# Optimization experiments

Measured on AMD Instinct MI355X. Metric: run time of the kernel, lower is better.

The kernel has to match this reference:

```python
import jax, jax.numpy as jnp
import numpy as np

N = 500_000
E = 16_000_000
G = 5_000
F_IN = 64
DIM = 10


def _mlp(x, W1, b1, W2, b2):
    return jnp.maximum(x @ W1 + b1, 0.0) @ W2 + b2


def setup_inputs() -> dict:
    key = jax.random.key(0)
    ks = jax.random.split(key, 32)
    inp = {
        "h": jax.random.normal(ks[0], (N, F_IN), dtype=jnp.float32),
        "src": jax.random.randint(ks[1], (E,), 0, N, dtype=jnp.int32),
        "dst": jax.random.randint(ks[2], (E,), 0, N, dtype=jnp.int32),
        "node_graph": jnp.sort(jax.random.randint(ks[3], (N,), 0, G, dtype=jnp.int32)),
    }
    k = 4
    for i in range(1, 6):
        d_in = F_IN if i == 1 else DIM
        inp[f"W1_{i}"] = jax.random.normal(ks[k], (d_in, DIM), dtype=jnp.float32) * 0.1; k += 1
        inp[f"b1_{i}"] = jnp.zeros((DIM,), dtype=jnp.float32)
        inp[f"W2_{i}"] = jax.random.normal(ks[k], (DIM, DIM), dtype=jnp.float32) * 0.1; k += 1
        inp[f"b2_{i}"] = jnp.zeros((DIM,), dtype=jnp.float32)
        inp[f"l_{i}"] = jax.random.normal(ks[k], (DIM, 1), dtype=jnp.float32) * 0.1; k += 1
    return inp


def reference(h, src, dst, node_graph,
              W1_1, b1_1, W2_1, b2_1, l_1,
              W1_2, b1_2, W2_2, b2_2, l_2,
              W1_3, b1_3, W2_3, b2_3, l_3,
              W1_4, b1_4, W2_4, b2_4, l_4,
              W1_5, b1_5, W2_5, b2_5, l_5):
    # GINConv with eps=0: out = MLP(h + sum_{j in N(i)} h_j), then outer ReLU
    def gin(x, W1, b1, W2, b2):
        agg = jax.ops.segment_sum(x[src], dst, num_segments=N)
        return jnp.maximum(_mlp(x + agg, W1, b1, W2, b2), 0.0)

    x1 = gin(h, W1_1, b1_1, W2_1, b2_1)
    x2 = gin(x1, W1_2, b1_2, W2_2, b2_2)
    x3 = gin(x2, W1_3, b1_3, W2_3, b2_3)
    x4 = gin(x3, W1_4, b1_4, W2_4, b2_4)
    x5 = gin(x4, W1_5, b1_5, W2_5, b2_5)

    counts = jax.ops.segment_sum(jnp.ones((N,), dtype=jnp.float32), node_graph, num_segments=G)
    counts = jnp.maximum(counts, 1.0)[:, None]  # [G,1]

    def mean_nodes(x):
        return jax.ops.segment_sum(x, node_graph, num_segments=G) / counts

    s = (mean_nodes(x1) @ l_1 + mean_nodes(x2) @ l_2 + mean_nodes(x3) @ l_3
         + mean_nodes(x4) @ l_4 + mean_nodes(x5) @ l_5)  # [G,1]
    return jax.nn.sigmoid(s)
```

## Files before the change

### kernel.cpp

```cpp
#include <hip/hip_runtime.h>


#define SENTINEL 0xFFFFFFFFu

__device__ __forceinline__ unsigned short f2bf(float f) {
    unsigned b = __float_as_uint(f);
    b += 0x7fffu + ((b >> 16) & 1u);
    return (unsigned short)(b >> 16);
}
__device__ __forceinline__ float bflo(unsigned u) { return __uint_as_float(u << 16); }
__device__ __forceinline__ float bfhi(unsigned u) { return __uint_as_float(u & 0xffff0000u); }

__global__ void k1_hw1_bf16(const float* __restrict__ h, const float* __restrict__ W1,
                            unsigned* __restrict__ y, int N) {
    __shared__ float sW[640];
    for (int i = threadIdx.x; i < 640; i += blockDim.x) sW[i] = W1[i];
    __syncthreads();
    int n = blockIdx.x * blockDim.x + threadIdx.x;
    if (n >= N) return;
    const float* hr = h + (size_t)n * 64;
    float acc[10];
#pragma unroll
    for (int j = 0; j < 10; j++) acc[j] = 0.f;
#pragma unroll 4
    for (int k = 0; k < 64; k += 4) {
        float4 hv = *(const float4*)(hr + k);
#pragma unroll
        for (int j = 0; j < 10; j++) {
            acc[j] += hv.x * sW[(k + 0) * 10 + j];
            acc[j] += hv.y * sW[(k + 1) * 10 + j];
            acc[j] += hv.z * sW[(k + 2) * 10 + j];
            acc[j] += hv.w * sW[(k + 3) * 10 + j];
        }
    }
    unsigned r0 = (unsigned)f2bf(acc[0]) | ((unsigned)f2bf(acc[1]) << 16);
    unsigned r1 = (unsigned)f2bf(acc[2]) | ((unsigned)f2bf(acc[3]) << 16);
    unsigned r2 = (unsigned)f2bf(acc[4]) | ((unsigned)f2bf(acc[5]) << 16);
    unsigned r3 = (unsigned)f2bf(acc[6]) | ((unsigned)f2bf(acc[7]) << 16);
    unsigned r4 = (unsigned)f2bf(acc[8]) | ((unsigned)f2bf(acc[9]) << 16);
    unsigned* yr = y + (size_t)n * 8;
    *(uint4*)yr = make_uint4(r0, r1, r2, r3);
    yr[4] = r4;
}

__global__ void k1_hw1_f32(const float* __restrict__ h, const float* __restrict__ W1,
                           float* __restrict__ y, int N) {
    __shared__ float sW[640];
    for (int i = threadIdx.x; i < 640; i += blockDim.x) sW[i] = W1[i];
    __syncthreads();
    int n = blockIdx.x * blockDim.x + threadIdx.x;
    if (n >= N) return;
    const float* hr = h + (size_t)n * 64;
    float acc[10];
#pragma unroll
    for (int j = 0; j < 10; j++) acc[j] = 0.f;
#pragma unroll 4
    for (int k = 0; k < 64; k += 4) {
        float4 hv = *(const float4*)(hr + k);
#pragma unroll
        for (int j = 0; j < 10; j++) {
            acc[j] += hv.x * sW[(k + 0) * 10 + j];
            acc[j] += hv.y * sW[(k + 1) * 10 + j];
            acc[j] += hv.z * sW[(k + 2) * 10 + j];
            acc[j] += hv.w * sW[(k + 3) * 10 + j];
        }
    }
    float* yr = y + (size_t)n * 16;
#pragma unroll
    for (int j = 0; j < 10; j++) yr[j] = acc[j];
}

__global__ void k_bhist(const int* __restrict__ dst, unsigned* __restrict__ bucket_cnt,
                        int E) {
    __shared__ unsigned h[512];
    int t = threadIdx.x;
    h[t] = 0; h[t + 256] = 0;
    __syncthreads();
    int stride = gridDim.x * blockDim.x;
    for (int e = blockIdx.x * blockDim.x + t; e < E; e += stride)
        atomicAdd(&h[(unsigned)dst[e] >> 10], 1u);
    __syncthreads();
    if (h[t]) atomicAdd(&bucket_cnt[t], h[t]);
    if (h[t + 256]) atomicAdd(&bucket_cnt[t + 256], h[t + 256]);
}

__global__ void k_bscan(const unsigned* __restrict__ bucket_cnt,
                        unsigned* __restrict__ bbase, unsigned* __restrict__ bcur, int B) {
    __shared__ unsigned s[512];
    int t = threadIdx.x;
    unsigned v = (t < B) ? bucket_cnt[t] : 0u;
    s[t] = v;
    __syncthreads();
    for (int off = 1; off < 512; off <<= 1) {
        unsigned u = (t >= off) ? s[t - off] : 0u;
        __syncthreads();
        s[t] += u;
        __syncthreads();
    }
    unsigned excl = s[t] - v;
    if (t < B) { bbase[t] = excl; bcur[t] = excl; }
    if (t == B - 1) bbase[B] = s[t];
}

__global__ __launch_bounds__(1024) void k_bscatter2(
        const int* __restrict__ src, const int* __restrict__ dst,
        unsigned* __restrict__ bcur, unsigned* __restrict__ pairs,
        int E, int nblocks) {
    __shared__ unsigned cnt[512];
    int t = threadIdx.x;
    int per = (E + nblocks - 1) / nblocks;
    int beg = blockIdx.x * per;
    int end = beg + per; if (end > E) end = E;
    if (beg >= E) return;
    if (t < 512) cnt[t] = 0;
    __syncthreads();
    for (int e = beg + t; e < end; e += 1024)
        atomicAdd(&cnt[(unsigned)dst[e] >> 10], 1u);
    __syncthreads();
    unsigned c = 0, base = 0;
    if (t < 512) { c = cnt[t]; if (c) base = atomicAdd(&bcur[t], c); }
    __syncthreads();
    if (t < 512) cnt[t] = base;
    __syncthreads();
    for (int e = beg + t; e < end; e += 1024) {
        unsigned d = (unsigned)dst[e];
        unsigned pos = atomicAdd(&cnt[d >> 10], 1u);
        pairs[pos] = ((unsigned)src[e] << 10) | (d & 1023u);
    }
}

__global__ __launch_bounds__(1024) void k_p2(
        const unsigned* __restrict__ pairs, const unsigned* __restrict__ bbase,
        unsigned* __restrict__ edges, unsigned* __restrict__ row_start,
        int N, int B, int E, int packed) {
    __shared__ unsigned cnt[1024], scn[1024], cur[1024];
    int t = threadIdx.x, b = blockIdx.x;
    unsigned beg = bbase[b], end = bbase[b + 1];
    cnt[t] = 0;
    __syncthreads();
    for (unsigned e = beg + t; e < end; e += 1024)
        atomicAdd(&cnt[pairs[e] & 1023u], 1u);
    __syncthreads();
    unsigned v = cnt[t];
    scn[t] = v;
    __syncthreads();
    for (int off = 1; off < 1024; off <<= 1) {
        unsigned u = (t >= off) ? scn[t - off] : 0u;
        __syncthreads();
        scn[t] += u;
        __syncthreads();
    }
    unsigned excl = scn[t] - v;
    int node = (b << 10) + t;
    if (node < N) row_start[node] = beg + excl;
    if (b == B - 1 && t == 0) row_start[N] = (unsigned)E;
    cur[t] = beg + excl;
    __syncthreads();
    for (unsigned e = beg + t; e < end; e += 1024) {
        unsigned pv = pairs[e];
        unsigned pos = atomicAdd(&cur[pv & 1023u], 1u);
        edges[pos] = packed ? pv : (pv >> 10);
    }
}

__global__ __launch_bounds__(256) void kA_agg(
        const unsigned* __restrict__ yin, const unsigned* __restrict__ epk,
        const unsigned* __restrict__ bbase,
        float* __restrict__ agg, float* __restrict__ carry_val,
        unsigned* __restrict__ carry_dst, int E, int B, int W) {
    __shared__ unsigned sb[513];
    for (int i = threadIdx.x; i < B + 1; i += 256) sb[i] = bbase[i];
    __syncthreads();
    int lane = threadIdx.x & 63;
    int w = blockIdx.x * 4 + (threadIdx.x >> 6);
    int e = (w << 6) + lane;
    bool v = e < E;
    float acc[10];
    unsigned dst;
    if (v) {
        unsigned pv = epk[e];
        unsigned s = pv >> 10;
        const unsigned* pr = yin + (size_t)s * 8;
        uint4 q = *(const uint4*)pr;
        unsigned q4 = pr[4];
        int lo = 0, hi = B - 1;
        while (lo < hi) { int m = (lo + hi + 1) >> 1; if (sb[m] <= (unsigned)e) lo = m; else hi = m - 1; }
        dst = ((unsigned)lo << 10) | (pv & 1023u);
        acc[0] = bflo(q.x); acc[1] = bfhi(q.x);
        acc[2] = bflo(q.y); acc[3] = bfhi(q.y);
        acc[4] = bflo(q.z); acc[5] = bfhi(q.z);
        acc[6] = bflo(q.w); acc[7] = bfhi(q.w);
        acc[8] = bflo(q4);  acc[9] = bfhi(q4);
    } else {
        dst = SENTINEL;
#pragma unroll
        for (int j = 0; j < 10; j++) acc[j] = 0.f;
    }
#pragma unroll
    for (int off = 1; off < 64; off <<= 1) {
        unsigned od = __shfl_up(dst, off);
        float tv[10];
#pragma unroll
        for (int j = 0; j < 10; j++) tv[j] = __shfl_up(acc[j], off);
        bool take = (lane >= off) && (od == dst);
#pragma unroll
        for (int j = 0; j < 10; j++) acc[j] = take ? acc[j] + tv[j] : acc[j];
    }
    unsigned dn = __shfl_down(dst, 1);
    bool is_end = (lane < 63) && (dst != dn);
    if (v && is_end) {
        float* ar = agg + (size_t)dst * 16;
        *(float4*)ar = make_float4(acc[0], acc[1], acc[2], acc[3]);
        *(float4*)(ar + 4) = make_float4(acc[4], acc[5], acc[6], acc[7]);
        *(float2*)(ar + 8) = make_float2(acc[8], acc[9]);
    }
    if (lane == 63 && w < W) {
        carry_dst[w] = dst;
        float* cr = carry_val + (size_t)w * 16;
        *(float4*)cr = make_float4(acc[0], acc[1], acc[2], acc[3]);
        *(float4*)(cr + 4) = make_float4(acc[4], acc[5], acc[6], acc[7]);
        *(float2*)(cr + 8) = make_float2(acc[8], acc[9]);
    }
}

__global__ __launch_bounds__(256) void kB_node(
        const unsigned* __restrict__ yin, unsigned* __restrict__ yout,
        const float* __restrict__ agg,
        const unsigned* __restrict__ row_start,
        const unsigned* __restrict__ carry_dst, const float* __restrict__ carry_val,
        const float* __restrict__ b1, const float* __restrict__ W2,
        const float* __restrict__ b2, const float* __restrict__ l,
        const float* __restrict__ W1n,
        const int* __restrict__ node_graph, float* __restrict__ gacc,
        int N, int last) {
    __shared__ float sW2[100], sW1[100], sb1[10], sb2[10], sl[10];
    int t = threadIdx.x;
    if (t < 100) sW2[t] = W2[t];
    if (!last && t >= 128 && t < 228) sW1[t - 128] = W1n[t - 128];
    if (t < 10) { sb1[t] = b1[t]; sb2[t] = b2[t]; sl[t] = l[t]; }
    __syncthreads();
    int n = blockIdx.x * 256 + t;
    bool valid = n < N;
    int nc = valid ? n : (N - 1);
    const unsigned* yr = yin + (size_t)nc * 8;
    uint4 q = *(const uint4*)yr;
    unsigned q4 = yr[4];
    float acc[10] = {bflo(q.x), bfhi(q.x), bflo(q.y), bfhi(q.y),
                     bflo(q.z), bfhi(q.z), bflo(q.w), bfhi(q.w),
                     bflo(q4),  bfhi(q4)};

    if (valid) {
        unsigned rs0 = row_start[n], rs1 = row_start[n + 1];
        if (rs1 > rs0) {
            unsigned le = rs1 - 1;
            if ((le & 63u) != 63u) {
                const float* ar = agg + (size_t)n * 16;
                float4 pa = *(const float4*)ar;
                float4 pb = *(const float4*)(ar + 4);
                float2 pc = *(const float2*)(ar + 8);
                acc[0] += pa.x; acc[1] += pa.y; acc[2] += pa.z; acc[3] += pa.w;
                acc[4] += pb.x; acc[5] += pb.y; acc[6] += pb.z; acc[7] += pb.w;
                acc[8] += pc.x; acc[9] += pc.y;
            }
            unsigned w0 = rs0 >> 6, w1 = le >> 6;
            for (unsigned w = w0; w <= w1; ++w) {
                if (carry_dst[w] == (unsigned)n) {
                    const float* cr = carry_val + (size_t)w * 16;
                    float4 pa = *(const float4*)cr;
                    float4 pb = *(const float4*)(cr + 4);
                    float2 pc = *(const float2*)(cr + 8);
                    acc[0] += pa.x; acc[1] += pa.y; acc[2] += pa.z; acc[3] += pa.w;
                    acc[4] += pb.x; acc[5] += pb.y; acc[6] += pb.z; acc[7] += pb.w;
                    acc[8] += pc.x; acc[9] += pc.y;
                }
            }
        }
    }

    float z[10], x[10];
#pragma unroll
    for (int j = 0; j < 10; j++) {
        float v = acc[j] + sb1[j];
        z[j] = v > 0.f ? v : 0.f;
    }
#pragma unroll
    for (int j = 0; j < 10; j++) {
        float v = sb2[j];
#pragma unroll
        for (int k = 0; k < 10; k++) v += z[k] * sW2[k * 10 + j];
        x[j] = v > 0.f ? v : 0.f;
    }
    float p = 0.f;
#pragma unroll
    for (int j = 0; j < 10; j++) p += x[j] * sl[j];
    if (!valid) p = 0.f;
    int g = node_graph[nc];

    int g0 = __shfl(g, 0);
    if (__all(g == g0)) {
#pragma unroll
        for (int off = 32; off > 0; off >>= 1) p += __shfl_down(p, off);
        if ((t & 63) == 0) unsafeAtomicAdd(&gacc[g0], p);
    } else {
        if (valid) unsafeAtomicAdd(&gacc[g], p);
    }

    if (!last && valid) {
        float yn[10];
#pragma unroll
        for (int j = 0; j < 10; j++) {
            float v = 0.f;
#pragma unroll
            for (int k = 0; k < 10; k++) v += x[k] * sW1[k * 10 + j];
            yn[j] = v;
        }
        unsigned r0 = (unsigned)f2bf(yn[0]) | ((unsigned)f2bf(yn[1]) << 16);
        unsigned r1 = (unsigned)f2bf(yn[2]) | ((unsigned)f2bf(yn[3]) << 16);
        unsigned r2 = (unsigned)f2bf(yn[4]) | ((unsigned)f2bf(yn[5]) << 16);
        unsigned r3 = (unsigned)f2bf(yn[6]) | ((unsigned)f2bf(yn[7]) << 16);
        unsigned r4 = (unsigned)f2bf(yn[8]) | ((unsigned)f2bf(yn[9]) << 16);
        unsigned* yo = yout + (size_t)n * 8;
        *(uint4*)yo = make_uint4(r0, r1, r2, r3);
        yo[4] = r4;
    }
}

__global__ void k4_final(const float* __restrict__ gacc, const int* __restrict__ node_graph,
                         float* __restrict__ out, int N, int G) {
    int g = blockIdx.x * blockDim.x + threadIdx.x;
    if (g >= G) return;
    int lo = 0, hi = N;
    while (lo < hi) { int m = (lo + hi) >> 1; if (node_graph[m] < g) lo = m + 1; else hi = m; }
    int lo2 = lo, hi2 = N;
    while (lo2 < hi2) { int m = (lo2 + hi2) >> 1; if (node_graph[m] <= g) lo2 = m + 1; else hi2 = m; }
    float c = (float)(hi2 - lo);
    if (c < 1.f) c = 1.f;
    float s = gacc[g] / c;
    out[g] = 1.f / (1.f + __expf(-s));
}

__global__ __launch_bounds__(256) void k_layer(
        const float* __restrict__ yin, float* __restrict__ yout,
        const unsigned* __restrict__ row_start, const unsigned* __restrict__ edges,
        const float* __restrict__ b1, const float* __restrict__ W2,
        const float* __restrict__ b2, const float* __restrict__ l,
        const float* __restrict__ W1n,
        const int* __restrict__ node_graph, float* __restrict__ gacc,
        int N, int last) {
    __shared__ float sW2[100], sW1[100], sb1[10], sb2[10], sl[10];
    int t = threadIdx.x;
    if (t < 100) sW2[t] = W2[t];
    if (!last && t >= 128 && t < 228) sW1[t - 128] = W1n[t - 128];
    if (t < 10) { sb1[t] = b1[t]; sb2[t] = b2[t]; sl[t] = l[t]; }
    __syncthreads();
    int n = blockIdx.x * 256 + t;
    bool valid = n < N;
    int nc = valid ? n : (N - 1);
    const float* yr = yin + (size_t)nc * 16;
    float4 a = *(const float4*)yr;
    float4 b = *(const float4*)(yr + 4);
    float2 c = *(const float2*)(yr + 8);
    float acc[10] = {a.x, a.y, a.z, a.w, b.x, b.y, b.z, b.w, c.x, c.y};
    unsigned beg = 0, end = 0;
    if (valid) { beg = row_start[n]; end = row_start[n + 1]; }
    for (unsigned e = beg; e < end; ++e) {
        unsigned s = edges[e];
        const float* pr = yin + (size_t)s * 16;
        float4 pa = *(const float4*)pr;
        float4 pb = *(const float4*)(pr + 4);
        float2 pc = *(const float2*)(pr + 8);
        acc[0] += pa.x; acc[1] += pa.y; acc[2] += pa.z; acc[3] += pa.w;
        acc[4] += pb.x; acc[5] += pb.y; acc[6] += pb.z; acc[7] += pb.w;
        acc[8] += pc.x; acc[9] += pc.y;
    }
    float z[10], x[10];
#pragma unroll
    for (int j = 0; j < 10; j++) {
        float v = acc[j] + sb1[j];
        z[j] = v > 0.f ? v : 0.f;
    }
#pragma unroll
    for (int j = 0; j < 10; j++) {
        float v = sb2[j];
#pragma unroll
        for (int k = 0; k < 10; k++) v += z[k] * sW2[k * 10 + j];
        x[j] = v > 0.f ? v : 0.f;
    }
    float p = 0.f;
#pragma unroll
    for (int j = 0; j < 10; j++) p += x[j] * sl[j];
    if (!valid) p = 0.f;
    int g = node_graph[nc];
    int g0 = __shfl(g, 0);
    if (__all(g == g0)) {
#pragma unroll
        for (int off = 32; off > 0; off >>= 1) p += __shfl_down(p, off);
        if ((t & 63) == 0) unsafeAtomicAdd(&gacc[g0], p);
    } else {
        if (valid) unsafeAtomicAdd(&gacc[g], p);
    }
    if (!last && valid) {
        float yn[10];
#pragma unroll
        for (int j = 0; j < 10; j++) {
            float v = 0.f;
#pragma unroll
            for (int k = 0; k < 10; k++) v += x[k] * sW1[k * 10 + j];
            yn[j] = v;
        }
        float* yo = yout + (size_t)n * 16;
        *(float4*)yo = make_float4(yn[0], yn[1], yn[2], yn[3]);
        *(float4*)(yo + 4) = make_float4(yn[4], yn[5], yn[6], yn[7]);
        *(float2*)(yo + 8) = make_float2(yn[8], yn[9]);
    }
}

static inline size_t al16(size_t w) { return (w + 15) & ~(size_t)15; }

extern "C" void kernel_launch(void* const* d_in, const int* in_sizes, int n_in,
                              void* d_out, int out_size, void* d_ws, size_t ws_size,
                              hipStream_t stream) {
    const float* h  = (const float*)d_in[0];
    const int* src  = (const int*)d_in[1];
    const int* dst  = (const int*)d_in[2];
    const int* ng   = (const int*)d_in[3];
    int N = in_sizes[3];
    int E = in_sizes[1];
    int G = out_size;

    const float* W1[5]; const float* b1[5]; const float* W2[5]; const float* b2[5]; const float* l[5];
    for (int i = 0; i < 5; i++) {
        W1[i] = (const float*)d_in[4 + i * 5 + 0];
        b1[i] = (const float*)d_in[4 + i * 5 + 1];
        W2[i] = (const float*)d_in[4 + i * 5 + 2];
        b2[i] = (const float*)d_in[4 + i * 5 + 3];
        l[i]  = (const float*)d_in[4 + i * 5 + 4];
    }
    float* out = (float*)d_out;

    int B = (N + 1023) >> 10;
    int W = (E + 63) >> 6;

    size_t wY   = al16((size_t)N * 8);
    size_t wRg2 = al16(((size_t)E > (size_t)N * 8) ? (size_t)E : (size_t)N * 8);
    size_t wE   = al16((size_t)E);
    size_t wRS  = al16((size_t)N + 1);
    size_t wAgg = al16((size_t)N * 16);
    size_t wCV  = al16((size_t)W * 16);
    size_t wCD  = al16((size_t)W);
    size_t need_r6 = (wY + wRg2 + wE + wRS + wAgg + wCV + wCD + 1552 + al16((size_t)G)) * 4;

    size_t regAB = (size_t)N * 16;
    size_t reg2f = ((size_t)E > regAB) ? (size_t)E : regAB;
    size_t need_r4 = (regAB + reg2f + (size_t)E + (size_t)(N + 1) + 1537 + (size_t)G) * 4;

    if (ws_size >= need_r6 && B <= 512) {
        unsigned* y0 = (unsigned*)d_ws;
        unsigned* pairs = y0 + wY;
        unsigned* y1 = pairs;
        unsigned* edges = pairs + wRg2;
        unsigned* row_start = edges + wE;
        float* agg = (float*)(row_start + wRS);
        float* carry_val = agg + wAgg;
        unsigned* carry_dst = (unsigned*)(carry_val + wCV);
        unsigned* bucket_cnt = carry_dst + wCD;
        unsigned* bbase = bucket_cnt + 512;
        unsigned* bcur = bbase + 513;
        float* gacc = (float*)(bcur + 512);

        hipMemsetAsync(bucket_cnt, 0, 512 * 4, stream);
        hipMemsetAsync(gacc, 0, (size_t)G * 4, stream);

        k1_hw1_bf16<<<(N + 255) / 256, 256, 0, stream>>>(h, W1[0], y0, N);

        k_bhist<<<2048, 256, 0, stream>>>(dst, bucket_cnt, E);
        k_bscan<<<1, 512, 0, stream>>>(bucket_cnt, bbase, bcur, B);
        k_bscatter2<<<256, 1024, 0, stream>>>(src, dst, bcur, pairs, E, 256);
        k_p2<<<B, 1024, 0, stream>>>(pairs, bbase, edges, row_start, N, B, E, 1);

        unsigned* ybuf[2] = {y0, y1};
        int ablocks = (W + 3) / 4;
        for (int i = 0; i < 5; i++) {
            kA_agg<<<ablocks, 256, 0, stream>>>(
                ybuf[i & 1], edges, bbase, agg, carry_val, carry_dst, E, B, W);
            kB_node<<<(N + 255) / 256, 256, 0, stream>>>(
                ybuf[i & 1], ybuf[(i + 1) & 1], agg, row_start, carry_dst, carry_val,
                b1[i], W2[i], b2[i], l[i], i < 4 ? W1[i + 1] : nullptr,
                ng, gacc, N, i == 4 ? 1 : 0);
        }
        k4_final<<<(G + 255) / 256, 256, 0, stream>>>(gacc, ng, out, N, G);
        return;
    }

    if (ws_size >= need_r4 && B <= 512) {
        float* y0 = (float*)d_ws;
        unsigned* pairs = (unsigned*)(y0 + regAB);
        float* y1 = (float*)pairs;
        unsigned* edges = pairs + reg2f;
        unsigned* row_start = edges + E;
        unsigned* bucket_cnt = row_start + (N + 1);
        unsigned* bbase = bucket_cnt + 512;
        unsigned* bcur = bbase + 513;
        float* gacc = (float*)(bcur + 512);

        hipMemsetAsync(bucket_cnt, 0, 512 * 4, stream);
        hipMemsetAsync(gacc, 0, (size_t)G * 4, stream);

        k1_hw1_f32<<<(N + 255) / 256, 256, 0, stream>>>(h, W1[0], y0, N);
        k_bhist<<<2048, 256, 0, stream>>>(dst, bucket_cnt, E);
        k_bscan<<<1, 512, 0, stream>>>(bucket_cnt, bbase, bcur, B);
        k_bscatter2<<<256, 1024, 0, stream>>>(src, dst, bcur, pairs, E, 256);
        k_p2<<<B, 1024, 0, stream>>>(pairs, bbase, edges, row_start, N, B, E, 0);

        float* ybuf[2] = {y0, y1};
        for (int i = 0; i < 5; i++) {
            k_layer<<<(N + 255) / 256, 256, 0, stream>>>(
                ybuf[i & 1], ybuf[(i + 1) & 1], row_start, edges,
                b1[i], W2[i], b2[i], l[i], i < 4 ? W1[i + 1] : nullptr,
                ng, gacc, N, i == 4 ? 1 : 0);
        }
        k4_final<<<(G + 255) / 256, 256, 0, stream>>>(gacc, ng, out, N, G);
    }
}
```

Measured before the change: 2.348 ms.

## Process two edges per lane in segmented-scan aggregation kernel

The edge aggregation kernel now handles two consecutive sorted edges per lane. It combines them locally when they share a destination, otherwise it writes the first one directly, and then runs the 64-lane segmented shuffle scan over 128-edge chunks. This halves the number of wavefronts and per-edge shuffle steps and also halves the carry array. The node kernel's carry and agg lookup logic is updated to the 128-edge windows, which adds extra boundary branching and a second shuffle pass whenever any lane holds an internal boundary.

```diff
diff --git a/kernel.cpp b/kernel.cpp
--- a/kernel.cpp
+++ b/kernel.cpp
@@ -167,59 +167,112 @@
         const unsigned* __restrict__ yin, const unsigned* __restrict__ epk,
         const unsigned* __restrict__ bbase,
         float* __restrict__ agg, float* __restrict__ carry_val,
-        unsigned* __restrict__ carry_dst, int E, int B, int W) {
+        unsigned* __restrict__ carry_dst, int E, int B, int W2) {
     __shared__ unsigned sb[513];
     for (int i = threadIdx.x; i < B + 1; i += 256) sb[i] = bbase[i];
     __syncthreads();
     int lane = threadIdx.x & 63;
     int w = blockIdx.x * 4 + (threadIdx.x >> 6);
-    int e = (w << 6) + lane;
-    bool v = e < E;
-    float acc[10];
-    unsigned dst;
-    if (v) {
-        unsigned pv = epk[e];
-        unsigned s = pv >> 10;
-        const unsigned* pr = yin + (size_t)s * 8;
-        uint4 q = *(const uint4*)pr;
-        unsigned q4 = pr[4];
+    int e0 = (w << 7) + (lane << 1);
+    int e1 = e0 + 1;
+    bool v0 = e0 < E, v1 = e1 < E;
+
+    unsigned dst0 = SENTINEL, sdst = SENTINEL, first_dst = SENTINEL;
+    bool internal = false;
+    float a0[10], sacc[10];
+#pragma unroll
+    for (int j = 0; j < 10; j++) { a0[j] = 0.f; sacc[j] = 0.f; }
+
+    if (v0) {
+        unsigned pv0, pv1 = 0;
+        if (v1) { uint2 pp = *(const uint2*)(epk + e0); pv0 = pp.x; pv1 = pp.y; }
+        else pv0 = epk[e0];
         int lo = 0, hi = B - 1;
-        while (lo < hi) { int m = (lo + hi + 1) >> 1; if (sb[m] <= (unsigned)e) lo = m; else hi = m - 1; }
-        dst = ((unsigned)lo << 10) | (pv & 1023u);
-        acc[0] = bflo(q.x); acc[1] = bfhi(q.x);
-        acc[2] = bflo(q.y); acc[3] = bfhi(q.y);
-        acc[4] = bflo(q.z); acc[5] = bfhi(q.z);
-        acc[6] = bflo(q.w); acc[7] = bfhi(q.w);
-        acc[8] = bflo(q4);  acc[9] = bfhi(q4);
-    } else {
-        dst = SENTINEL;
-#pragma unroll
-        for (int j = 0; j < 10; j++) acc[j] = 0.f;
-    }
+        while (lo < hi) { int m = (lo + hi + 1) >> 1; if (sb[m] <= (unsigned)e0) lo = m; else hi = m - 1; }
+        dst0 = ((unsigned)lo << 10) | (pv0 & 1023u);
+        first_dst = dst0;
+        const unsigned* p0 = yin + (size_t)(pv0 >> 10) * 8;
+        uint4 q0 = *(const uint4*)p0;
+        unsigned q04 = p0[4];
+        float r0[10] = {bflo(q0.x), bfhi(q0.x), bflo(q0.y), bfhi(q0.y),
+                        bflo(q0.z), bfhi(q0.z), bflo(q0.w), bfhi(q0.w),
+                        bflo(q04),  bfhi(q04)};
+        if (v1) {
+            int b1 = lo;
+            while (b1 < B - 1 && sb[b1 + 1] <= (unsigned)e1) b1++;
+            unsigned dst1 = ((unsigned)b1 << 10) | (pv1 & 1023u);
+            const unsigned* p1 = yin + (size_t)(pv1 >> 10) * 8;
+            uint4 q1 = *(const uint4*)p1;
+            unsigned q14 = p1[4];
+            float r1[10] = {bflo(q1.x), bfhi(q1.x), bflo(q1.y), bfhi(q1.y),
+                            bflo(q1.z), bfhi(q1.z), bflo(q1.w), bfhi(q1.w),
+                            bflo(q14),  bfhi(q14)};
+            if (dst1 == dst0) {
+                sdst = dst0;
+#pragma unroll
+                for (int j = 0; j < 10; j++) sacc[j] = r0[j] + r1[j];
+            } else {
+                internal = true;
+                sdst = dst1;
+#pragma unroll
+                for (int j = 0; j < 10; j++) { a0[j] = r0[j]; sacc[j] = r1[j]; }
+            }
+        } else {
+            sdst = dst0;
+#pragma unroll
+            for (int j = 0; j < 10; j++) sacc[j] = r0[j];
+        }
+    }
+
 #pragma unroll
     for (int off = 1; off < 64; off <<= 1) {
-        unsigned od = __shfl_up(dst, off);
+        unsigned od = __shfl_up(sdst, off);
         float tv[10];
 #pragma unroll
-        for (int j = 0; j < 10; j++) tv[j] = __shfl_up(acc[j], off);
-        bool take = (lane >= off) && (od == dst);
-#pragma unroll
-        for (int j = 0; j < 10; j++) acc[j] = take ? acc[j] + tv[j] : acc[j];
-    }
-    unsigned dn = __shfl_down(dst, 1);
-    bool is_end = (lane < 63) && (dst != dn);
-    if (v && is_end) {
-        float* ar = agg + (size_t)dst * 16;
-        *(float4*)ar = make_float4(acc[0], acc[1], acc[2], acc[3]);
-        *(float4*)(ar + 4) = make_float4(acc[4], acc[5], acc[6], acc[7]);
-        *(float2*)(ar + 8) = make_float2(acc[8], acc[9]);
-    }
-    if (lane == 63 && w < W) {
-        carry_dst[w] = dst;
+        for (int j = 0; j < 10; j++) tv[j] = __shfl_up(sacc[j], off);
+        bool take = (lane >= off) && (od == sdst);
+#pragma unroll
+        for (int j = 0; j < 10; j++) sacc[j] = take ? sacc[j] + tv[j] : sacc[j];
+    }
+
+    if (__any(internal)) {
+        unsigned pdst = __shfl_up(sdst, 1);
+        float pacc[10];
+#pragma unroll
+        for (int j = 0; j < 10; j++) pacc[j] = __shfl_up(sacc[j], 1);
+        if (internal) {
+            bool ci = (lane > 0) && (pdst == dst0);
+            float* ar = agg + (size_t)dst0 * 16;
+            float t0 = a0[0] + (ci ? pacc[0] : 0.f);
+            float t1 = a0[1] + (ci ? pacc[1] : 0.f);
+            float t2 = a0[2] + (ci ? pacc[2] : 0.f);
+            float t3 = a0[3] + (ci ? pacc[3] : 0.f);
+            float t4 = a0[4] + (ci ? pacc[4] : 0.f);
+            float t5 = a0[5] + (ci ? pacc[5] : 0.f);
+            float t6 = a0[6] + (ci ? pacc[6] : 0.f);
+            float t7 = a0[7] + (ci ? pacc[7] : 0.f);
+            float t8 = a0[8] + (ci ? pacc[8] : 0.f);
+            float t9 = a0[9] + (ci ? pacc[9] : 0.f);
+            *(float4*)ar = make_float4(t0, t1, t2, t3);
+            *(float4*)(ar + 4) = make_float4(t4, t5, t6, t7);
+            *(float2*)(ar + 8) = make_float2(t8, t9);
+        }
+    }
+
+    unsigned nfirst = __shfl_down(first_dst, 1);
+    bool is_end = (lane < 63) && (sdst != nfirst);
+    if (v0 && is_end) {
+        float* ar = agg + (size_t)sdst * 16;
+        *(float4*)ar = make_float4(sacc[0], sacc[1], sacc[2], sacc[3]);
+        *(float4*)(ar + 4) = make_float4(sacc[4], sacc[5], sacc[6], sacc[7]);
+        *(float2*)(ar + 8) = make_float2(sacc[8], sacc[9]);
+    }
+    if (lane == 63 && w < W2) {
+        carry_dst[w] = sdst;
         float* cr = carry_val + (size_t)w * 16;
-        *(float4*)cr = make_float4(acc[0], acc[1], acc[2], acc[3]);
-        *(float4*)(cr + 4) = make_float4(acc[4], acc[5], acc[6], acc[7]);
-        *(float2*)(cr + 8) = make_float2(acc[8], acc[9]);
+        *(float4*)cr = make_float4(sacc[0], sacc[1], sacc[2], sacc[3]);
+        *(float4*)(cr + 4) = make_float4(sacc[4], sacc[5], sacc[6], sacc[7]);
+        *(float2*)(cr + 8) = make_float2(sacc[8], sacc[9]);
     }
 }
 
@@ -232,7 +285,7 @@
         const float* __restrict__ b2, const float* __restrict__ l,
         const float* __restrict__ W1n,
         const int* __restrict__ node_graph, float* __restrict__ gacc,
-        int N, int last) {
+        int N, int E, int last) {
     __shared__ float sW2[100], sW1[100], sb1[10], sb2[10], sl[10];
     int t = threadIdx.x;
     if (t < 100) sW2[t] = W2[t];
@@ -253,7 +306,9 @@
         unsigned rs0 = row_start[n], rs1 = row_start[n + 1];
         if (rs1 > rs0) {
             unsigned le = rs1 - 1;
-            if ((le & 63u) != 63u) {
+            bool carry_only = ((le & 127u) == 127u) ||
+                              ((le == (unsigned)(E - 1)) && ((le & 127u) == 126u));
+            if (!carry_only) {
                 const float* ar = agg + (size_t)n * 16;
                 float4 pa = *(const float4*)ar;
                 float4 pb = *(const float4*)(ar + 4);
@@ -262,7 +317,7 @@
                 acc[4] += pb.x; acc[5] += pb.y; acc[6] += pb.z; acc[7] += pb.w;
                 acc[8] += pc.x; acc[9] += pc.y;
             }
-            unsigned w0 = rs0 >> 6, w1 = le >> 6;
+            unsigned w0 = rs0 >> 7, w1 = le >> 7;
             for (unsigned w = w0; w <= w1; ++w) {
                 if (carry_dst[w] == (unsigned)n) {
                     const float* cr = carry_val + (size_t)w * 16;
@@ -439,22 +494,22 @@
     float* out = (float*)d_out;
 
     int B = (N + 1023) >> 10;
-    int W = (E + 63) >> 6;
+    int W2n = (E + 127) >> 7;
 
     size_t wY   = al16((size_t)N * 8);
     size_t wRg2 = al16(((size_t)E > (size_t)N * 8) ? (size_t)E : (size_t)N * 8);
     size_t wE   = al16((size_t)E);
     size_t wRS  = al16((size_t)N + 1);
     size_t wAgg = al16((size_t)N * 16);
-    size_t wCV  = al16((size_t)W * 16);
-    size_t wCD  = al16((size_t)W);
-    size_t need_r6 = (wY + wRg2 + wE + wRS + wAgg + wCV + wCD + 1552 + al16((size_t)G)) * 4;
+    size_t wCV  = al16((size_t)W2n * 16);
+    size_t wCD  = al16((size_t)W2n);
+    size_t need_r7 = (wY + wRg2 + wE + wRS + wAgg + wCV + wCD + 1552 + al16((size_t)G)) * 4;
 
     size_t regAB = (size_t)N * 16;
     size_t reg2f = ((size_t)E > regAB) ? (size_t)E : regAB;
     size_t need_r4 = (regAB + reg2f + (size_t)E + (size_t)(N + 1) + 1537 + (size_t)G) * 4;
 
-    if (ws_size >= need_r6 && B <= 512) {
+    if (ws_size >= need_r7 && B <= 512) {
         unsigned* y0 = (unsigned*)d_ws;
         unsigned* pairs = y0 + wY;
         unsigned* y1 = pairs;
@@ -479,14 +534,14 @@
         k_p2<<<B, 1024, 0, stream>>>(pairs, bbase, edges, row_start, N, B, E, 1);
 
         unsigned* ybuf[2] = {y0, y1};
-        int ablocks = (W + 3) / 4;
+        int ablocks = (W2n + 3) / 4;
         for (int i = 0; i < 5; i++) {
             kA_agg<<<ablocks, 256, 0, stream>>>(
-                ybuf[i & 1], edges, bbase, agg, carry_val, carry_dst, E, B, W);
+                ybuf[i & 1], edges, bbase, agg, carry_val, carry_dst, E, B, W2n);
             kB_node<<<(N + 255) / 256, 256, 0, stream>>>(
                 ybuf[i & 1], ybuf[(i + 1) & 1], agg, row_start, carry_dst, carry_val,
                 b1[i], W2[i], b2[i], l[i], i < 4 ? W1[i + 1] : nullptr,
-                ng, gacc, N, i == 4 ? 1 : 0);
+                ng, gacc, N, E, i == 4 ? 1 : 0);
         }
         k4_final<<<(G + 255) / 256, 256, 0, stream>>>(gacc, ng, out, N, G);
         return;
```

After: 2.300 ms. 1.02x faster.
